# Kernel tuning notes

Hardware: AMD Instinct MI355X
Metric: run time of the kernel (lower is better)

The kernel has to match this reference:

```python
import jax, jax.numpy as jnp
import numpy as np

D_MODEL = 512
SEQ_LEN = 512
H = 8
D_K = D_MODEL // H  # 64
SCALE = 1.0 / float(np.sqrt(D_K))


def setup_inputs() -> dict:
    key = jax.random.key(0)
    ks = jax.random.split(key, 6)
    x_q = jax.random.normal(ks[0], (1, SEQ_LEN, D_MODEL), dtype=jnp.float32)
    x_k = jax.random.normal(ks[1], (1, SEQ_LEN, D_MODEL), dtype=jnp.float32)
    attention_mask = jnp.ones((1, SEQ_LEN), dtype=jnp.float32)
    # xavier-uniform-like init scale
    def xav(k, shape):
        lim = float(np.sqrt(6.0 / (shape[0] + shape[1])))
        return jax.random.uniform(k, shape, jnp.float32, -lim, lim)
    W_Q = xav(ks[2], (D_MODEL, D_K))
    W_K = xav(ks[3], (D_MODEL, D_K))
    W_V = xav(ks[4], (D_MODEL, D_K))
    W_O = xav(ks[5], (H * D_K, D_MODEL))
    return {"x_q": x_q, "x_k": x_k, "attention_mask": attention_mask,
            "W_Q": W_Q, "W_K": W_K, "W_V": W_V, "W_O": W_O}


def reference(x_q, x_k, attention_mask, W_Q, W_K, W_V, W_O):
    # Single-head attention (the original reuses the same W_Q/W_K/W_V for all 8 heads).
    Q = jnp.einsum('bsd,dk->bsk', x_q, W_Q)          # [1,S,64]
    K = jnp.einsum('bsd,dk->bsk', x_k, W_K)          # [1,S,64]
    V = jnp.einsum('bsd,dv->bsv', x_k, W_V)          # [1,S,64]
    # has_mask=False: causal_mask = ones(1,S,S) * attention_mask[:,None,:]
    mask = jnp.ones((1, SEQ_LEN, SEQ_LEN), dtype=x_q.dtype) * attention_mask[:, None, :]
    scores = SCALE * jnp.einsum('bsk,btk->bst', Q, K)  # [1,S,S]
    scores = jnp.where(mask == 0, -jnp.inf, scores)
    sm = jax.nn.softmax(scores, axis=-1)
    head = jnp.einsum('bst,btv->bsv', sm, V)         # [1,S,64]
    # All 8 heads are identical -> concatenation == tiling along feature dim.
    heads = jnp.tile(head, (1, 1, H))                 # [1,S,512]
    return heads @ W_O                                # [1,S,512]
```

## Files before the change

### kernel.cpp

```cpp
#include <hip/hip_runtime.h>
#include <hip/hip_fp16.h>
#include <math.h>

#define SEQ 512
#define DM  512
#define DK  64
#define NH  8
#define SCALE 0.125f

#define F4FOLD(a, off) { a.x += __shfl_xor(a.x, off, 64); a.y += __shfl_xor(a.y, off, 64); \
                         a.z += __shfl_xor(a.z, off, 64); a.w += __shfl_xor(a.w, off, 64); }
#define F4FMA(acc, s, v) { acc.x += (s)*(v).x; acc.y += (s)*(v).y; \
                           acc.z += (s)*(v).z; acc.w += (s)*(v).w; }

__global__ __launch_bounds__(512) void qkv_wor_kernel(
    const float* __restrict__ xq, const float* __restrict__ xk,
    const float* __restrict__ WQ, const float* __restrict__ WK,
    const float* __restrict__ WV, const float* __restrict__ WO,
    float* __restrict__ Q, __half* __restrict__ Kh,
    __half* __restrict__ Vh, __half* __restrict__ Worh)
{
    const int b   = blockIdx.x;
    const int rg  = b >> 1;
    const int kh  = b & 1;
    const int tid = threadIdx.x;
    const int r0  = 4 * rg;

    __shared__ __align__(16) float xq_s[4][DM], xk_s[4][DM];
    __shared__ __align__(16) float part_s[3][8][4][32];

    reinterpret_cast<float4*>(xq_s)[tid] =
        reinterpret_cast<const float4*>(xq + r0 * DM)[tid];
    reinterpret_cast<float4*>(xk_s)[tid] =
        reinterpret_cast<const float4*>(xk + r0 * DM)[tid];
    __syncthreads();

    const int w     = tid >> 6;
    const int l     = tid & 63;
    const int drow  = l >> 3;
    const int kq    = (l & 7) * 4;
    const int kbase = kh * 32;

    float4 aq[4] = {}, ak[4] = {}, av[4] = {};
    #pragma unroll
    for (int it = 0; it < 8; ++it) {
        const int d = w * 64 + it * 8 + drow;
        const float4 wq = *reinterpret_cast<const float4*>(WQ + d * DK + kbase + kq);
        const float4 wk = *reinterpret_cast<const float4*>(WK + d * DK + kbase + kq);
        const float4 wv = *reinterpret_cast<const float4*>(WV + d * DK + kbase + kq);
        #pragma unroll
        for (int r = 0; r < 4; ++r) {
            const float xqr = xq_s[r][d];
            const float xkr = xk_s[r][d];
            F4FMA(aq[r], xqr, wq);
            F4FMA(ak[r], xkr, wk);
            F4FMA(av[r], xkr, wv);
        }
    }
    #pragma unroll
    for (int off = 8; off < 64; off <<= 1) {
        #pragma unroll
        for (int r = 0; r < 4; ++r) {
            F4FOLD(aq[r], off); F4FOLD(ak[r], off); F4FOLD(av[r], off);
        }
    }
    if (l < 8) {
        #pragma unroll
        for (int r = 0; r < 4; ++r) {
            *reinterpret_cast<float4*>(&part_s[0][w][r][kq]) = aq[r];
            *reinterpret_cast<float4*>(&part_s[1][w][r][kq]) = ak[r];
            *reinterpret_cast<float4*>(&part_s[2][w][r][kq]) = av[r];
        }
    }
    __syncthreads();

    if (tid < 384) {
        const int m   = tid >> 7;
        const int rem = tid & 127;
        const int r   = rem >> 5;
        const int k   = rem & 31;
        float s = 0.f;
        #pragma unroll
        for (int p = 0; p < 8; ++p) s += part_s[m][p][r][k];
        const int gi = (r0 + r) * DK + kbase + k;
        if      (m == 0) Q[gi]  = s;
        else if (m == 1) Kh[gi] = __float2half_rn(s);
        else             Vh[gi] = __float2half_rn(s);
    } else {
        const int flat = b * 128 + (tid - 384);
        const int v = flat >> 9, d = flat & 511;
        float acc = 0.f;
        #pragma unroll
        for (int h = 0; h < NH; ++h) acc += WO[(h * DK + v) * DM + d];
        Worh[flat] = __float2half_rn(acc);
    }
}

__global__ __launch_bounds__(512) void attn_out_kernel(
    const float* __restrict__ Q, const __half* __restrict__ Kh,
    const __half* __restrict__ Vh, const __half* __restrict__ Worh,
    const float* __restrict__ amask, float* __restrict__ out)
{
    const int r0   = 2 * blockIdx.x;
    const int tid  = threadIdx.x;
    const int lane = tid & 63;
    const int w    = tid >> 6;
    const int dsub = lane >> 4;
    const int kq   = (lane & 15) * 4;

    __shared__ __align__(16) float q_s[2][DK];
    __shared__ __align__(16) float hpart_s[2][8][DK];
    __shared__ float psum_s[2][8];
    __shared__ __align__(16) float head_s[2][DK];

    float4 kreg[8];
    {
        const float4* k4 = reinterpret_cast<const float4*>(Kh + tid * DK);
        #pragma unroll
        for (int c = 0; c < 8; ++c) kreg[c] = k4[c];
    }
    if (tid < 2 * DK / 4)
        reinterpret_cast<float4*>(q_s)[tid] =
            reinterpret_cast<const float4*>(Q + r0 * DK)[tid];
    const float am = amask[tid];
    __syncthreads();

    float sc0 = 0.f, sc1 = 0.f;
    #pragma unroll
    for (int c = 0; c < 8; ++c) {
        const __half2* h2 = reinterpret_cast<const __half2*>(&kreg[c]);
        #pragma unroll
        for (int j = 0; j < 4; ++j) {
            const float2 kf = __half22float2(h2[j]);
            const int idx = c * 8 + j * 2;
            sc0 += q_s[0][idx] * kf.x + q_s[0][idx + 1] * kf.y;
            sc1 += q_s[1][idx] * kf.x + q_s[1][idx + 1] * kf.y;
        }
    }
    const float p0 = (am == 0.f) ? 0.f : __expf(sc0 * SCALE);
    const float p1 = (am == 0.f) ? 0.f : __expf(sc1 * SCALE);

    float4 h0{0,0,0,0}, h1{0,0,0,0};
    float ps0 = 0.f, ps1 = 0.f;
    #pragma unroll
    for (int it = 0; it < 16; ++it) {
        const int src = it * 4 + dsub;
        const int t   = w * 64 + src;
        const float pa = __shfl(p0, src, 64);
        const float pb = __shfl(p1, src, 64);
        const __half2* v2 = reinterpret_cast<const __half2*>(Vh + t * DK + kq);
        const float2 va = __half22float2(v2[0]);
        const float2 vb = __half22float2(v2[1]);
        h0.x += pa*va.x; h0.y += pa*va.y; h0.z += pa*vb.x; h0.w += pa*vb.y;
        h1.x += pb*va.x; h1.y += pb*va.y; h1.z += pb*vb.x; h1.w += pb*vb.y;
        ps0 += pa; ps1 += pb;
    }
    #pragma unroll
    for (int off = 16; off < 64; off <<= 1) {
        F4FOLD(h0, off); F4FOLD(h1, off);
        ps0 += __shfl_xor(ps0, off, 64);
        ps1 += __shfl_xor(ps1, off, 64);
    }
    if (dsub == 0) {
        *reinterpret_cast<float4*>(&hpart_s[0][w][kq]) = h0;
        *reinterpret_cast<float4*>(&hpart_s[1][w][kq]) = h1;
        if (lane == 0) { psum_s[0][w] = ps0; psum_s[1][w] = ps1; }
    }
    __syncthreads();

    if (tid < 2 * DK) {
        const int r = tid >> 6, k = tid & 63;
        float hs = 0.f, den = 0.f;
        #pragma unroll
        for (int p = 0; p < 8; ++p) { hs += hpart_s[r][p][k]; den += psum_s[r][p]; }
        head_s[r][k] = hs / den;
    }
    __syncthreads();

    if (tid < 256) {
        const int r  = tid >> 7;
        const int dq = tid & 127;
        float4 o{0,0,0,0};
        #pragma unroll 8
        for (int v = 0; v < DK; ++v) {
            const __half2* w2 = reinterpret_cast<const __half2*>(Worh + v * DM + dq * 4);
            const float2 a = __half22float2(w2[0]);
            const float2 c = __half22float2(w2[1]);
            const float hh = head_s[r][v];
            o.x += hh*a.x; o.y += hh*a.y; o.z += hh*c.x; o.w += hh*c.y;
        }
        reinterpret_cast<float4*>(out)[(r0 + r) * (DM/4) + dq] = o;
    }
}

extern "C" void kernel_launch(void* const* d_in, const int* in_sizes, int n_in,
                              void* d_out, int out_size, void* d_ws, size_t ws_size,
                              hipStream_t stream) {
    const float* xq    = (const float*)d_in[0];
    const float* xk    = (const float*)d_in[1];
    const float* amask = (const float*)d_in[2];
    const float* WQ    = (const float*)d_in[3];
    const float* WK    = (const float*)d_in[4];
    const float* WV    = (const float*)d_in[5];
    const float* WO    = (const float*)d_in[6];
    float* out = (float*)d_out;

    float*  ws   = (float*)d_ws;
    float*  Q    = ws;
    __half* Kh   = (__half*)(ws + 32768);
    __half* Vh   = (__half*)(ws + 32768 + 16384);
    __half* Worh = (__half*)(ws + 32768 + 32768);

    qkv_wor_kernel<<<SEQ/2, 512, 0, stream>>>(xq, xk, WQ, WK, WV, WO, Q, Kh, Vh, Worh);
    attn_out_kernel<<<SEQ/2, 512, 0, stream>>>(Q, Kh, Vh, Worh, amask, out);
}
```

Measured before the change: 20.88 us.

## Double attention block to 1024 threads, one query row per half, split-K output projection

The attention/output kernel now launches 1024 threads per block. Each 512-thread half handles one of the two query rows instead of every thread computing both. The output projection is split four ways over the value dimension, with partial sums reduced through shared memory, so all threads take part instead of only 256. This is meant to shorten per-thread serial work and raise latency hiding. In exchange, each block loads K twice, adds an extra reduction and barrier, and its larger size may limit how many blocks fit per CU.

After: 22.15 us. +6.1%, slower.

```diff
diff --git a/kernel.cpp b/kernel.cpp
--- a/kernel.cpp
+++ b/kernel.cpp
@@ -38,16 +38,16 @@
     const int w     = tid >> 6;
     const int l     = tid & 63;
     const int drow  = l >> 3;
-    const int kq    = (l & 7) * 4;
+    const int kq1   = (l & 7) * 4;
     const int kbase = kh * 32;
 
     float4 aq[4] = {}, ak[4] = {}, av[4] = {};
     #pragma unroll
     for (int it = 0; it < 8; ++it) {
         const int d = w * 64 + it * 8 + drow;
-        const float4 wq = *reinterpret_cast<const float4*>(WQ + d * DK + kbase + kq);
-        const float4 wk = *reinterpret_cast<const float4*>(WK + d * DK + kbase + kq);
-        const float4 wv = *reinterpret_cast<const float4*>(WV + d * DK + kbase + kq);
+        const float4 wq = *reinterpret_cast<const float4*>(WQ + d * DK + kbase + kq1);
+        const float4 wk = *reinterpret_cast<const float4*>(WK + d * DK + kbase + kq1);
+        const float4 wv = *reinterpret_cast<const float4*>(WV + d * DK + kbase + kq1);
         #pragma unroll
         for (int r = 0; r < 4; ++r) {
             const float xqr = xq_s[r][d];
@@ -67,9 +67,9 @@
     if (l < 8) {
         #pragma unroll
         for (int r = 0; r < 4; ++r) {
-            *reinterpret_cast<float4*>(&part_s[0][w][r][kq]) = aq[r];
-            *reinterpret_cast<float4*>(&part_s[1][w][r][kq]) = ak[r];
-            *reinterpret_cast<float4*>(&part_s[2][w][r][kq]) = av[r];
+            *reinterpret_cast<float4*>(&part_s[0][w][r][kq1]) = aq[r];
+            *reinterpret_cast<float4*>(&part_s[1][w][r][kq1]) = ak[r];
+            *reinterpret_cast<float4*>(&part_s[2][w][r][kq1]) = av[r];
         }
     }
     __syncthreads();
@@ -96,7 +96,7 @@
     }
 }
 
-__global__ __launch_bounds__(512) void attn_out_kernel(
+__global__ __launch_bounds__(1024) void attn_out_kernel(
     const float* __restrict__ Q, const __half* __restrict__ Kh,
     const __half* __restrict__ Vh, const __half* __restrict__ Worh,
     const float* __restrict__ amask, float* __restrict__ out)
@@ -105,6 +105,9 @@
     const int tid  = threadIdx.x;
     const int lane = tid & 63;
     const int w    = tid >> 6;
+    const int wl   = w & 7;
+    const int r    = tid >> 9;
+    const int t    = tid & 511;
     const int dsub = lane >> 4;
     const int kq   = (lane & 15) * 4;
 
@@ -112,20 +115,21 @@
     __shared__ __align__(16) float hpart_s[2][8][DK];
     __shared__ float psum_s[2][8];
     __shared__ __align__(16) float head_s[2][DK];
+    __shared__ __align__(16) float4 epi_s[4][2][DM/4];
 
     float4 kreg[8];
     {
-        const float4* k4 = reinterpret_cast<const float4*>(Kh + tid * DK);
+        const float4* k4 = reinterpret_cast<const float4*>(Kh + t * DK);
         #pragma unroll
         for (int c = 0; c < 8; ++c) kreg[c] = k4[c];
     }
     if (tid < 2 * DK / 4)
         reinterpret_cast<float4*>(q_s)[tid] =
             reinterpret_cast<const float4*>(Q + r0 * DK)[tid];
-    const float am = amask[tid];
-    __syncthreads();
-
-    float sc0 = 0.f, sc1 = 0.f;
+    const float am = amask[t];
+    __syncthreads();
+
+    float sc = 0.f;
     #pragma unroll
     for (int c = 0; c < 8; ++c) {
         const __half2* h2 = reinterpret_cast<const __half2*>(&kreg[c]);
@@ -133,63 +137,71 @@
         for (int j = 0; j < 4; ++j) {
             const float2 kf = __half22float2(h2[j]);
             const int idx = c * 8 + j * 2;
-            sc0 += q_s[0][idx] * kf.x + q_s[0][idx + 1] * kf.y;
-            sc1 += q_s[1][idx] * kf.x + q_s[1][idx + 1] * kf.y;
-        }
-    }
-    const float p0 = (am == 0.f) ? 0.f : __expf(sc0 * SCALE);
-    const float p1 = (am == 0.f) ? 0.f : __expf(sc1 * SCALE);
-
-    float4 h0{0,0,0,0}, h1{0,0,0,0};
-    float ps0 = 0.f, ps1 = 0.f;
+            sc += q_s[r][idx] * kf.x + q_s[r][idx + 1] * kf.y;
+        }
+    }
+    const float p = (am == 0.f) ? 0.f : __expf(sc * SCALE);
+
+    float4 h{0,0,0,0};
+    float ps = 0.f;
     #pragma unroll
     for (int it = 0; it < 16; ++it) {
         const int src = it * 4 + dsub;
-        const int t   = w * 64 + src;
-        const float pa = __shfl(p0, src, 64);
-        const float pb = __shfl(p1, src, 64);
-        const __half2* v2 = reinterpret_cast<const __half2*>(Vh + t * DK + kq);
+        const int tt  = wl * 64 + src;
+        const float pa = __shfl(p, src, 64);
+        const __half2* v2 = reinterpret_cast<const __half2*>(Vh + tt * DK + kq);
         const float2 va = __half22float2(v2[0]);
         const float2 vb = __half22float2(v2[1]);
-        h0.x += pa*va.x; h0.y += pa*va.y; h0.z += pa*vb.x; h0.w += pa*vb.y;
-        h1.x += pb*va.x; h1.y += pb*va.y; h1.z += pb*vb.x; h1.w += pb*vb.y;
-        ps0 += pa; ps1 += pb;
+        h.x += pa * va.x; h.y += pa * va.y; h.z += pa * vb.x; h.w += pa * vb.y;
+        ps  += pa;
     }
     #pragma unroll
     for (int off = 16; off < 64; off <<= 1) {
-        F4FOLD(h0, off); F4FOLD(h1, off);
-        ps0 += __shfl_xor(ps0, off, 64);
-        ps1 += __shfl_xor(ps1, off, 64);
+        F4FOLD(h, off);
+        ps += __shfl_xor(ps, off, 64);
     }
     if (dsub == 0) {
-        *reinterpret_cast<float4*>(&hpart_s[0][w][kq]) = h0;
-        *reinterpret_cast<float4*>(&hpart_s[1][w][kq]) = h1;
-        if (lane == 0) { psum_s[0][w] = ps0; psum_s[1][w] = ps1; }
+        *reinterpret_cast<float4*>(&hpart_s[r][wl][kq]) = h;
+        if (lane == 0) psum_s[r][wl] = ps;
     }
     __syncthreads();
 
     if (tid < 2 * DK) {
-        const int r = tid >> 6, k = tid & 63;
+        const int rr = tid >> 6, k = tid & 63;
         float hs = 0.f, den = 0.f;
         #pragma unroll
-        for (int p = 0; p < 8; ++p) { hs += hpart_s[r][p][k]; den += psum_s[r][p]; }
-        head_s[r][k] = hs / den;
-    }
-    __syncthreads();
-
-    if (tid < 256) {
-        const int r  = tid >> 7;
-        const int dq = tid & 127;
+        for (int p8 = 0; p8 < 8; ++p8) { hs += hpart_s[rr][p8][k]; den += psum_s[rr][p8]; }
+        head_s[rr][k] = hs / den;
+    }
+    __syncthreads();
+
+    {
+        const int rem = tid & 511;
+        const int dq  = rem & 127;
+        const int vq  = rem >> 7;
         float4 o{0,0,0,0};
-        #pragma unroll 8
-        for (int v = 0; v < DK; ++v) {
+        #pragma unroll
+        for (int j = 0; j < 16; ++j) {
+            const int v = vq * 16 + j;
             const __half2* w2 = reinterpret_cast<const __half2*>(Worh + v * DM + dq * 4);
             const float2 a = __half22float2(w2[0]);
             const float2 c = __half22float2(w2[1]);
             const float hh = head_s[r][v];
-            o.x += hh*a.x; o.y += hh*a.y; o.z += hh*c.x; o.w += hh*c.y;
-        }
-        reinterpret_cast<float4*>(out)[(r0 + r) * (DM/4) + dq] = o;
+            o.x += hh * a.x; o.y += hh * a.y; o.z += hh * c.x; o.w += hh * c.y;
+        }
+        epi_s[vq][r][dq] = o;
+    }
+    __syncthreads();
+    if (tid < 256) {
+        const int rr = tid >> 7, dq = tid & 127;
+        const float4 a = epi_s[0][rr][dq], b2 = epi_s[1][rr][dq];
+        const float4 c = epi_s[2][rr][dq], d2 = epi_s[3][rr][dq];
+        float4 o;
+        o.x = a.x + b2.x + c.x + d2.x;
+        o.y = a.y + b2.y + c.y + d2.y;
+        o.z = a.z + b2.z + c.z + d2.z;
+        o.w = a.w + b2.w + c.w + d2.w;
+        reinterpret_cast<float4*>(out)[(r0 + rr) * (DM/4) + dq] = o;
     }
 }
 
@@ -212,5 +224,5 @@
     __half* Worh = (__half*)(ws + 32768 + 32768);
 
     qkv_wor_kernel<<<SEQ/2, 512, 0, stream>>>(xq, xk, WQ, WK, WV, WO, Q, Kh, Vh, Worh);
-    attn_out_kernel<<<SEQ/2, 512, 0, stream>>>(Q, Kh, Vh, Worh, amask, out);
+    attn_out_kernel<<<SEQ/2, 1024, 0, stream>>>(Q, Kh, Vh, Worh, amask, out);
 }
```
